# Kernel optimization log

Hardware: AMD Instinct MI355X
Metric: run time of the kernel (lower is better)

## Reference

```python
import jax, jax.numpy as jnp
import numpy as np

B, N = 4, 20                        # batch, qubits
L = int(np.ceil(np.log2(N)))        # 5 layers, one 4x4 generator each


def setup_inputs():
    key = jax.random.key(0)
    k1, k2, k3, k4 = jax.random.split(key, 4)
    psi_re = jax.random.normal(k1, (B, 2 ** N), dtype=jnp.float32)
    psi_im = jax.random.normal(k2, (B, 2 ** N), dtype=jnp.float32)
    nrm = jnp.sqrt(jnp.sum(psi_re ** 2 + psi_im ** 2, axis=1, keepdims=True))
    psi_re, psi_im = psi_re / nrm, psi_im / nrm   # normalized quantum state
    H_re = jax.random.normal(k3, (L, 4, 4), dtype=jnp.float32)
    H_im = jax.random.normal(k4, (L, 4, 4), dtype=jnp.float32)
    return {"psi_re": psi_re, "psi_im": psi_im, "H_re": H_re, "H_im": H_im}


def _make_unitary(A):
    # torch.matrix_exp(A - A^H): expm of an anti-Hermitian generator via eigh
    G = A - A.conj().T
    w, V = jnp.linalg.eigh(-1j * G)            # G = i * Hermitian
    return (V * jnp.exp(1j * w)) @ V.conj().T  # expm(G), unitary


def _apply_gate(T, U4, axes):
    # contract 4x4 gate (reshaped [2,2,2,2]) onto two qubit axes of tensor T
    T = jnp.tensordot(U4, T, axes=((2, 3), axes))
    return jnp.moveaxis(T, (0, 1), axes)


def _gate_pairs(nq):
    pairs = [(2 * i, 2 * i + 1) for i in range(nq // 2)]
    if nq > 2:
        pairs += [(2 * i + 1, (2 * i + 2) % nq) for i in range(nq // 2)]
    return pairs


def _forward(psi_re, psi_im, H_re, H_im):
    psi = (psi_re + 1j * psi_im).astype(jnp.complex64).reshape((B,) + (2,) * N)
    H = (H_re + 1j * H_im).astype(jnp.complex64)
    state, is_dm, nq = psi, False, N
    for layer in range(L):
        U = _make_unitary(H[layer]).reshape(2, 2, 2, 2)
        Uc = U.conj()
        # _2local_conv: brick pattern of the same 2-qubit gate
        for (a, b) in _gate_pairs(nq):
            state = _apply_gate(state, U, (1 + a, 1 + b))
            if is_dm:  # density matrix: also apply U* on bra axes
                state = _apply_gate(state, Uc, (1 + nq + a, 1 + nq + b))
        # _2local_pool: measuring qubits 0..nq//2-1 with index shifting removes
        # the even-indexed qubits -> partial trace over them
        if nq >= 2:
            traced = [2 * i for i in range(nq // 2)]
            kept = [q for q in range(nq) if q not in traced]
            t, k = len(traced), len(kept)
            if is_dm:
                perm = (0,) + tuple(1 + q for q in kept) + tuple(1 + q for q in traced) \
                     + tuple(1 + nq + q for q in kept) + tuple(1 + nq + q for q in traced)
                r = jnp.transpose(state, perm).reshape(B, 2 ** k, 2 ** t, 2 ** k, 2 ** t)
                state = jnp.einsum('bitjt->bij', r).reshape((B,) + (2,) * k + (2,) * k)
            else:
                perm = (0,) + tuple(1 + q for q in traced) + tuple(1 + q for q in kept)
                p = jnp.transpose(state, perm).reshape(B, 2 ** t, 2 ** k)
                state = jnp.einsum('bti,btj->bij', p, p.conj()).reshape((B,) + (2,) * k + (2,) * k)
                is_dm = True
            nq = k
    # final state.measure(0): reduced 1-qubit density matrix, take P(outcome 0)
    r = state.reshape(B, 2, 2 ** (nq - 1), 2, 2 ** (nq - 1))
    rho0 = jnp.einsum('birjr->bij', r)
    return rho0[:, 0, 0].real


def reference(psi_re, psi_im, H_re, H_im):
    return _forward(psi_re, psi_im, H_re, H_im)
```

## Files before the change

### kernel.cpp

```cpp
#include <hip/hip_runtime.h>
#include <math.h>


typedef float cpx __attribute__((ext_vector_type(2)));

__device__ __forceinline__ cpx mkc(float x, float y) { cpx r; r.x = x; r.y = y; return r; }

__device__ __forceinline__ cpx cmul(cpx a, cpx b) {
  cpx r = a.xx * b;
  return __builtin_elementwise_fma(mkc(-a.y, a.y), b.yx, r);
}
__device__ __forceinline__ cpx cmadd(cpx acc, cpx a, cpx b) {
  acc = __builtin_elementwise_fma(a.xx, b, acc);
  return __builtin_elementwise_fma(mkc(-a.y, a.y), b.yx, acc);
}
__device__ __forceinline__ cpx cmaddc(cpx acc, cpx a, cpx b) {
  acc = __builtin_elementwise_fma(a.xx, mkc(b.x, -b.y), acc);
  return __builtin_elementwise_fma(a.yy, b.yx, acc);
}

__device__ __forceinline__ int pad(int e) { return e + (e >> 4); }
__device__ __forceinline__ int ins(int x, int p) {
  return ((x >> p) << (p + 1)) | (x & ((1 << p) - 1));
}

#define S_STR 36
#define T_STR 1153

__device__ __forceinline__ void gate4(cpx& v0, cpx& v1, cpx& v2, cpx& v3,
                                      const cpx (&U)[16]) {
  cpx n0 = cmul(U[0], v0);  n0 = cmadd(n0, U[1], v1);  n0 = cmadd(n0, U[2], v2);  n0 = cmadd(n0, U[3], v3);
  cpx n1 = cmul(U[4], v0);  n1 = cmadd(n1, U[5], v1);  n1 = cmadd(n1, U[6], v2);  n1 = cmadd(n1, U[7], v3);
  cpx n2 = cmul(U[8], v0);  n2 = cmadd(n2, U[9], v1);  n2 = cmadd(n2, U[10], v2); n2 = cmadd(n2, U[11], v3);
  cpx n3 = cmul(U[12], v0); n3 = cmadd(n3, U[13], v1); n3 = cmadd(n3, U[14], v2); n3 = cmadd(n3, U[15], v3);
  v0 = n0; v1 = n1; v2 = n2; v3 = n3;
}

template <int NG>
__device__ __forceinline__ void gate16n(cpx (&v)[16], const cpx (&U)[16]) {
#pragma unroll
  for (int g = 0; g < 4; g++)
    gate4(v[g * 4 + 0], v[g * 4 + 1], v[g * 4 + 2], v[g * 4 + 3], U);
#pragma unroll
  for (int lo = 0; lo < 4; lo++)
    gate4(v[lo], v[lo + 4], v[lo + 8], v[lo + 12], U);
  if (NG == 3) {
#pragma unroll
    for (int b3 = 0; b3 < 2; b3++)
#pragma unroll
      for (int b0 = 0; b0 < 2; b0++) {
        int j = b3 * 8 + b0;
        gate4(v[j], v[j + 2], v[j + 4], v[j + 6], U);
      }
  }
}

__device__ __forceinline__ void apply_gate_tile13(cpx* t, const cpx (&U)[16],
                                                  int pa, int pb, int tid) {
  int p0 = pa < pb ? pa : pb;
  int p1 = pa < pb ? pb : pa;
  int m0 = (1 << p0) - 1, m1 = (1 << p1) - 1;
  int ia = 1 << pa, ib = 1 << pb;
#pragma unroll
  for (int g = tid; g < 2048; g += 512) {
    int idx = ((g & ~m0) << 1) | (g & m0);
    idx = ((idx & ~m1) << 1) | (idx & m1);
    int e0 = pad(idx), e1 = pad(idx | ib), e2 = pad(idx | ia), e3 = pad(idx | ia | ib);
    cpx v0 = t[e0], v1 = t[e1], v2 = t[e2], v3 = t[e3];
    gate4(v0, v1, v2, v3, U);
    t[e0] = v0; t[e1] = v1; t[e2] = v2; t[e3] = v3;
  }
}

template <int NG>
__device__ __forceinline__ void phase4_f(cpx* t, const cpx (&U)[16],
                                         int q0, int q1, int q2, int q3,
                                         int o0, int o1, int o2, int o3, int tid) {
  int idx = ins(ins(ins(ins(tid, q0), q1), q2), q3);
  cpx v[16];
#pragma unroll
  for (int j = 0; j < 16; j++) {
    int off = ((j & 1) ? o0 : 0) + ((j & 2) ? o1 : 0) + ((j & 4) ? o2 : 0) + ((j & 8) ? o3 : 0);
    v[j] = t[pad(idx + off)];
  }
  gate16n<NG>(v, U);
#pragma unroll
  for (int j = 0; j < 16; j++) {
    int off = ((j & 1) ? o0 : 0) + ((j & 2) ? o1 : 0) + ((j & 4) ? o2 : 0) + ((j & 8) ? o3 : 0);
    t[pad(idx + off)] = v[j];
  }
}

template <int NG>
__device__ __forceinline__ void phase4_pool(cpx* w, const cpx (&U)[16],
                                            int a_lo, int a_hi, int c_lo, int c_hi,
                                            int o0, int o1, int o2, int o3, int tid) {
  int uu = tid & 7, ss = (tid >> 3) & 7, t_lo = tid >> 6;
  int u = ins(ins(uu, a_lo), a_hi);
  int s = ins(ins(ss, c_lo), c_hi);
  int base = t_lo * T_STR + s * S_STR + u;
  cpx v[16];
#pragma unroll
  for (int j = 0; j < 16; j++) {
    int off = ((j & 1) ? o0 : 0) + ((j & 2) ? o1 : 0) + ((j & 4) ? o2 : 0) + ((j & 8) ? o3 : 0);
    v[j] = w[base + off];
  }
  gate16n<NG>(v, U);
#pragma unroll
  for (int j = 0; j < 16; j++) {
    int off = ((j & 1) ? o0 : 0) + ((j & 2) ? o1 : 0) + ((j & 4) ? o2 : 0) + ((j & 8) ? o3 : 0);
    w[base + off] = v[j];
  }
}

__device__ __forceinline__ void pool_p3(cpx* w, const cpx (&U)[16], int tid) {
#pragma unroll
  for (int it = 0; it < 2; it++) {
    int h = tid + it * 512;
    int t_lo = h & 7, ss = (h >> 3) & 15, uu = (h >> 7) & 7;
    int base = t_lo * T_STR + (ss << 1) * S_STR + (uu << 2);
    cpx v[8];
    v[0] = w[base];          v[1] = w[base + 1];
    v[4] = w[base + 2];      v[5] = w[base + 3];
    v[2] = w[base + S_STR];      v[3] = w[base + S_STR + 1];
    v[6] = w[base + S_STR + 2];  v[7] = w[base + S_STR + 3];
    gate4(v[0], v[1], v[2], v[3], U);
    gate4(v[4], v[5], v[6], v[7], U);
    gate4(v[0], v[2], v[4], v[6], U);
    gate4(v[1], v[3], v[5], v[7], U);
    w[base] = v[0];          w[base + 1] = v[1];
    w[base + 2] = v[4];      w[base + 3] = v[5];
    w[base + S_STR] = v[2];      w[base + S_STR + 1] = v[3];
    w[base + S_STR + 2] = v[6];  w[base + S_STR + 3] = v[7];
  }
}

__device__ __forceinline__ cpx expm16(const float* __restrict__ Hre,
                                      const float* __restrict__ Him,
                                      int l, int l16) {
  int r = l16 >> 2, c = l16 & 3;
  double tr = (double)Hre[l * 16 + r * 4 + c] - (double)Hre[l * 16 + c * 4 + r];
  double ti = (double)Him[l * 16 + r * 4 + c] + (double)Him[l * 16 + c * 4 + r];
  double a = sqrt(tr * tr + ti * ti);
  a += __shfl_xor(a, 1, 16);
  a += __shfl_xor(a, 2, 16);
  double nrm = fmax(a, __shfl_xor(a, 4, 16));
  nrm = fmax(nrm, __shfl_xor(nrm, 8, 16));
  int s = 0;
  while (nrm > 0.25 && s < 60) { nrm *= 0.5; s++; }
  double sc = ldexp(1.0, -s);
  tr *= sc; ti *= sc;
  double id = (r == c) ? 1.0 : 0.0;
  double er = id, ei = 0.0, pr = id, pi = 0.0;
  for (int k = 1; k <= 16; k++) {
    double qr = 0.0, qi = 0.0;
#pragma unroll
    for (int m = 0; m < 4; m++) {
      double pmr = __shfl(pr, r * 4 + m, 16);
      double pmi = __shfl(pi, r * 4 + m, 16);
      double tmr = __shfl(tr, m * 4 + c, 16);
      double tmi = __shfl(ti, m * 4 + c, 16);
      qr = fma(pmr, tmr, fma(-pmi, tmi, qr));
      qi = fma(pmr, tmi, fma(pmi, tmr, qi));
    }
    double inv = 1.0 / (double)k;
    pr = qr * inv; pi = qi * inv;
    er += pr; ei += pi;
  }
  for (int it = 0; it < s; it++) {
    double qr = 0.0, qi = 0.0;
#pragma unroll
    for (int m = 0; m < 4; m++) {
      double amr = __shfl(er, r * 4 + m, 16);
      double ami = __shfl(ei, r * 4 + m, 16);
      double bmr = __shfl(er, m * 4 + c, 16);
      double bmi = __shfl(ei, m * 4 + c, 16);
      qr = fma(amr, bmr, fma(-ami, bmi, qr));
      qi = fma(amr, bmi, fma(ami, bmr, qi));
    }
    er = qr; ei = qi;
  }
  return mkc((float)er, (float)ei);
}

__global__ __launch_bounds__(512, 4) void l0_pass1(const float* __restrict__ pre,
                                                   const float* __restrict__ pim,
                                                   const float* __restrict__ Hre,
                                                   const float* __restrict__ Him,
                                                   cpx* __restrict__ Umat,
                                                   cpx* __restrict__ state) {
  extern __shared__ cpx tile[];
  __shared__ cpx Ush[16];
  int tid = threadIdx.x;
  int bid = blockIdx.x;
  int b = bid >> 7, hi = bid & 127;
  size_t base = ((size_t)b << 20) | ((size_t)hi << 13);
  float4 re[4], im[4];
#pragma unroll
  for (int k = 0; k < 4; k++) {
    int e = (tid + (k << 9)) << 2;
    re[k] = *(const float4*)&pre[base + e];
    im[k] = *(const float4*)&pim[base + e];
  }
#pragma unroll
  for (int k = 0; k < 4; k++) {
    int e = (tid + (k << 9)) << 2;
    int d = pad(e);
    tile[d]     = mkc(re[k].x, im[k].x);
    tile[d + 1] = mkc(re[k].y, im[k].y);
    tile[d + 2] = mkc(re[k].z, im[k].z);
    tile[d + 3] = mkc(re[k].w, im[k].w);
  }
  {
    int wv = tid >> 6, g16 = (tid & 63) >> 4, l16 = tid & 15;
    int layer = (wv == 0) ? g16 : ((wv == 1 && g16 == 0) ? 4 : -1);
    if (layer == 0 || (bid == 0 && layer > 0)) {
      cpx ue = expm16(Hre, Him, layer, l16);
      if (layer == 0) Ush[l16] = ue;
      if (bid == 0) Umat[layer * 16 + l16] = ue;
    }
  }
  __syncthreads();
  cpx U[16];
#pragma unroll
  for (int k = 0; k < 16; k++) U[k] = Ush[k];
  phase4_f<3>(tile, U, 0, 1, 2, 3, 1, 2, 4, 8, tid);            __syncthreads();
  phase4_f<3>(tile, U, 4, 5, 6, 7, 16, 32, 64, 128, tid);       __syncthreads();
  phase4_f<3>(tile, U, 8, 9, 10, 11, 256, 512, 1024, 2048, tid);__syncthreads();
  phase4_f<2>(tile, U, 3, 4, 7, 8, 8, 16, 128, 256, tid);       __syncthreads();
  int hifix = ((hi & 1) << 16) | (((hi >> 1) & 1) << 6) | (((hi >> 2) & 1) << 17)
            | (((hi >> 3) & 1) << 5) | (((hi >> 4) & 1) << 18) | (((hi >> 5) & 1) << 7)
            | (((hi >> 6) & 1) << 19);
  size_t dbase = ((size_t)b << 20) | (unsigned)hifix;
  cpx x[16];
#pragma unroll
  for (int k = 0; k < 4; k++) {
    int src = pad((tid + (k << 9)) << 2);
    x[4 * k + 0] = tile[src];     x[4 * k + 1] = tile[src + 1];
    x[4 * k + 2] = tile[src + 2]; x[4 * k + 3] = tile[src + 3];
  }
#pragma unroll
  for (int k = 0; k < 4; k++) {
    int le = tid + (k << 9);
    int d = ((le & 1) << 2) | (((le >> 1) & 1) << 3) | (((le >> 2) & 1) << 8)
          | (((le >> 3) & 1) << 12) | (((le >> 4) & 1) << 10) | (((le >> 5) & 1) << 13)
          | (((le >> 6) & 1) << 9) | (((le >> 7) & 1) << 14) | (((le >> 8) & 1) << 11)
          | (((le >> 9) & 1) << 15) | (((le >> 10) & 1) << 4);
    float4* dst = (float4*)&state[dbase + d];
    dst[0] = make_float4(x[4 * k].x, x[4 * k].y, x[4 * k + 1].x, x[4 * k + 1].y);
    dst[1] = make_float4(x[4 * k + 2].x, x[4 * k + 2].y, x[4 * k + 3].x, x[4 * k + 3].y);
  }
}

__global__ __launch_bounds__(512, 4) void l0_pass2(const cpx* __restrict__ Umat,
                                                   cpx* __restrict__ state) {
  extern __shared__ cpx tile[];
  int tid = threadIdx.x;
  int bid = blockIdx.x;
  int b = bid >> 7, mid = bid & 127;
  size_t base = ((size_t)b << 20) | ((size_t)mid << 8);
  cpx U[16];
#pragma unroll
  for (int k = 0; k < 16; k++) U[k] = Umat[k];
  {
    float4 v[8];
#pragma unroll
    for (int k = 0; k < 8; k++) {
      int f = tid + (k << 9);
      int run = f >> 7, idx = f & 127;
      v[k] = *(const float4*)&state[base + ((size_t)run << 15) + ((size_t)idx << 1)];
    }
#pragma unroll
    for (int k = 0; k < 8; k++) {
      int f = tid + (k << 9);
      int d = pad((f >> 7) * 256 + (f & 127) * 2);
      tile[d] = mkc(v[k].x, v[k].y);
      tile[d + 1] = mkc(v[k].z, v[k].w);
    }
  }
  __syncthreads();
  phase4_f<3>(tile, U, 4, 6, 9, 10, 16, 512, 64, 1024, tid);    __syncthreads();
  phase4_f<3>(tile, U, 5, 7, 11, 12, 32, 2048, 128, 4096, tid); __syncthreads();
  phase4_f<2>(tile, U, 4, 5, 8, 10, 256, 16, 1024, 32, tid);    __syncthreads();
  apply_gate_tile13(tile, U, 0, 12, tid);                       __syncthreads();
  {
    cpx y[16];
#pragma unroll
    for (int k = 0; k < 8; k++) {
      int f = tid + (k << 9);
      int d = pad((f >> 7) * 256 + (f & 127) * 2);
      y[2 * k] = tile[d];
      y[2 * k + 1] = tile[d + 1];
    }
#pragma unroll
    for (int k = 0; k < 8; k++) {
      int f = tid + (k << 9);
      int run = f >> 7, idx = f & 127;
      size_t a = base + ((size_t)run << 15) + ((size_t)idx << 1);
      *(float4*)&state[a] = make_float4(y[2 * k].x, y[2 * k].y, y[2 * k + 1].x, y[2 * k + 1].y);
    }
  }
}

__global__ __launch_bounds__(512, 4) void pool_l1(const cpx* __restrict__ Umat,
                                                  const cpx* __restrict__ state,
                                                  float4* __restrict__ partial) {
  extern __shared__ cpx w[];
  int tid = threadIdx.x;
  int bid = blockIdx.x;
  int b = bid >> 7, thi = bid & 127;
  size_t base = ((size_t)b << 20) | ((size_t)thi << 13);
  cpx U[16];
#pragma unroll
  for (int k = 0; k < 16; k++) U[k] = Umat[16 + k];
  {
    float4 v[8];
#pragma unroll
    for (int k = 0; k < 8; k++) {
      int e = (tid + (k << 9)) << 1;
      v[k] = *(const float4*)&state[base + e];
    }
#pragma unroll
    for (int k = 0; k < 8; k++) {
      int e = (tid + (k << 9)) << 1;
      int u = (((e >> 8) & 1) << 1) | (((e >> 9) & 1) << 2) | (((e >> 4) & 1) << 3) | (((e >> 5) & 1) << 4);
      int s = ((e >> 2) & 1) | (((e >> 10) & 1) << 1) | (((e >> 11) & 1) << 2)
            | (((e >> 6) & 1) << 3) | (((e >> 7) & 1) << 4);
      int t = ((e >> 1) & 1) | (((e >> 3) & 1) << 1) | (((e >> 12) & 1) << 2);
      int c = t * T_STR + s * S_STR + u;
      w[c] = mkc(v[k].x, v[k].y);
      w[c + 1] = mkc(v[k].z, v[k].w);
    }
  }
  __syncthreads();
  phase4_pool<3>(w, U, 3, 4, 3, 4, 8, 8 * S_STR, 16, 16 * S_STR, tid); __syncthreads();
  phase4_pool<3>(w, U, 1, 2, 1, 2, 2, 2 * S_STR, 4, 4 * S_STR, tid);   __syncthreads();
  pool_p3(w, U, tid);                                                  __syncthreads();
  phase4_pool<2>(w, U, 0, 3, 2, 4, 4 * S_STR, 8, 16 * S_STR, 1, tid);  __syncthreads();
  int wv = tid >> 6, lane = tid & 63;
  int u0 = (lane >> 3) << 2, v0 = (lane & 7) << 2;
  cpx acc[4][4];
#pragma unroll
  for (int i = 0; i < 4; i++)
#pragma unroll
    for (int j = 0; j < 4; j++) acc[i][j] = mkc(0.f, 0.f);
  {
    int tb = wv * T_STR;
#pragma unroll 4
    for (int s = 0; s < 32; s++) {
      int row = tb + s * S_STR;
      cpx x[4], y[4];
#pragma unroll
      for (int i = 0; i < 4; i++) { x[i] = w[row + u0 + i]; y[i] = w[row + v0 + i]; }
#pragma unroll
      for (int i = 0; i < 4; i++)
#pragma unroll
        for (int j = 0; j < 4; j++) acc[i][j] = cmaddc(acc[i][j], x[i], y[j]);
    }
  }
  __syncthreads();
#pragma unroll
  for (int i = 0; i < 4; i++)
#pragma unroll
    for (int j = 0; j < 4; j++)
      w[wv * 1024 + (u0 + i) * 32 + (v0 + j)] = acc[i][j];
  __syncthreads();
  {
    cpx s0 = mkc(0.f, 0.f), s1 = mkc(0.f, 0.f);
#pragma unroll
    for (int k = 0; k < 8; k++) {
      s0 += w[k * 1024 + 2 * tid];
      s1 += w[k * 1024 + 2 * tid + 1];
    }
    partial[((size_t)bid << 9) | tid] = make_float4(s0.x, s0.y, s1.x, s1.y);
  }
}

__global__ __launch_bounds__(256) void finish(const cpx* __restrict__ Umat,
                                              const float4* __restrict__ accv,
                                              float* __restrict__ out) {
  __shared__ cpx rho[1024];
  __shared__ cpx r3s[64];
  __shared__ cpx r4s[16];
  int tid = threadIdx.x;
  int b = blockIdx.x;
  float4* rf = (float4*)rho;
  for (int f = tid; f < 512; f += 256) {
    float4 acc = make_float4(0.f, 0.f, 0.f, 0.f);
#pragma unroll 8
    for (int h = 0; h < 128; h++) {
      float4 v = accv[(size_t)(b * 128 + h) * 512 + f];
      acc.x += v.x; acc.y += v.y; acc.z += v.z; acc.w += v.w;
    }
    rf[f] = acc;
  }
  __syncthreads();

  cpx U[16], Uc[16];
#pragma unroll
  for (int k = 0; k < 16; k++) { U[k] = Umat[32 + k]; Uc[k] = mkc(U[k].x, -U[k].y); }
  const int gl2[4][2] = {{4,3},{2,1},{3,2},{1,0}};
#pragma unroll
  for (int gi = 0; gi < 4; gi++) {
    int pa = gl2[gi][0], pb = gl2[gi][1];
    int p0 = pa < pb ? pa : pb, p1 = pa < pb ? pb : pa;
    int m0 = (1 << p0) - 1, m1 = (1 << p1) - 1;
    int ia = 1 << pa, ib = 1 << pb;
    {
      int j = tid >> 3, g = tid & 7;
      int idx = ((g & ~m0) << 1) | (g & m0);
      idx = ((idx & ~m1) << 1) | (idx & m1);
      cpx v0 = rho[idx * 32 + j], v1 = rho[(idx | ib) * 32 + j];
      cpx v2 = rho[(idx | ia) * 32 + j], v3 = rho[(idx | ia | ib) * 32 + j];
      gate4(v0, v1, v2, v3, U);
      rho[idx * 32 + j] = v0; rho[(idx | ib) * 32 + j] = v1;
      rho[(idx | ia) * 32 + j] = v2; rho[(idx | ia | ib) * 32 + j] = v3;
    }
    __syncthreads();
    {
      int i = tid >> 3, g = tid & 7;
      int idx = ((g & ~m0) << 1) | (g & m0);
      idx = ((idx & ~m1) << 1) | (idx & m1);
      cpx v0 = rho[i * 32 + idx], v1 = rho[i * 32 + (idx | ib)];
      cpx v2 = rho[i * 32 + (idx | ia)], v3 = rho[i * 32 + (idx | ia | ib)];
      gate4(v0, v1, v2, v3, Uc);
      rho[i * 32 + idx] = v0; rho[i * 32 + (idx | ib)] = v1;
      rho[i * 32 + (idx | ia)] = v2; rho[i * 32 + (idx | ia | ib)] = v3;
    }
    __syncthreads();
  }
  if (tid < 64) {
    int u = tid >> 3, v = tid & 7;
    cpx acc = mkc(0.f, 0.f);
#pragma unroll
    for (int s = 0; s < 4; s++) {
      int iu = ((s >> 1) << 4) | ((u >> 2) << 3) | ((s & 1) << 2) | (((u >> 1) & 1) << 1) | (u & 1);
      int iv = ((s >> 1) << 4) | ((v >> 2) << 3) | ((s & 1) << 2) | (((v >> 1) & 1) << 1) | (v & 1);
      cpx x = rho[iu * 32 + iv];
      acc.x += x.x; acc.y += x.y;
    }
    r3s[u * 8 + v] = acc;
  }
  __syncthreads();

#pragma unroll
  for (int k = 0; k < 16; k++) { U[k] = Umat[48 + k]; Uc[k] = mkc(U[k].x, -U[k].y); }
  const int gl3[2][2] = {{2,1},{1,0}};
#pragma unroll
  for (int gi = 0; gi < 2; gi++) {
    int pa = gl3[gi][0], pb = gl3[gi][1];
    int p0 = pa < pb ? pa : pb, p1 = pa < pb ? pb : pa;
    int m0 = (1 << p0) - 1, m1 = (1 << p1) - 1;
    int ia = 1 << pa, ib = 1 << pb;
    if (tid < 16) {
      int j = tid >> 1, g = tid & 1;
      int idx = ((g & ~m0) << 1) | (g & m0);
      idx = ((idx & ~m1) << 1) | (idx & m1);
      cpx v0 = r3s[idx * 8 + j], v1 = r3s[(idx | ib) * 8 + j];
      cpx v2 = r3s[(idx | ia) * 8 + j], v3 = r3s[(idx | ia | ib) * 8 + j];
      gate4(v0, v1, v2, v3, U);
      r3s[idx * 8 + j] = v0; r3s[(idx | ib) * 8 + j] = v1;
      r3s[(idx | ia) * 8 + j] = v2; r3s[(idx | ia | ib) * 8 + j] = v3;
    }
    __syncthreads();
    if (tid < 16) {
      int i = tid >> 1, g = tid & 1;
      int idx = ((g & ~m0) << 1) | (g & m0);
      idx = ((idx & ~m1) << 1) | (idx & m1);
      cpx v0 = r3s[i * 8 + idx], v1 = r3s[i * 8 + (idx | ib)];
      cpx v2 = r3s[i * 8 + (idx | ia)], v3 = r3s[i * 8 + (idx | ia | ib)];
      gate4(v0, v1, v2, v3, Uc);
      r3s[i * 8 + idx] = v0; r3s[i * 8 + (idx | ib)] = v1;
      r3s[i * 8 + (idx | ia)] = v2; r3s[i * 8 + (idx | ia | ib)] = v3;
    }
    __syncthreads();
  }
  if (tid < 16) {
    int u = tid >> 2, v = tid & 3;
    cpx acc = mkc(0.f, 0.f);
#pragma unroll
    for (int s = 0; s < 2; s++) {
      cpx x = r3s[((s << 2) | u) * 8 + ((s << 2) | v)];
      acc.x += x.x; acc.y += x.y;
    }
    r4s[u * 4 + v] = acc;
  }
  __syncthreads();

#pragma unroll
  for (int k = 0; k < 16; k++) { U[k] = Umat[64 + k]; Uc[k] = mkc(U[k].x, -U[k].y); }
  if (tid < 4) {
    int j = tid;
    cpx v0 = r4s[0 * 4 + j], v1 = r4s[1 * 4 + j], v2 = r4s[2 * 4 + j], v3 = r4s[3 * 4 + j];
    gate4(v0, v1, v2, v3, U);
    r4s[0 * 4 + j] = v0; r4s[1 * 4 + j] = v1; r4s[2 * 4 + j] = v2; r4s[3 * 4 + j] = v3;
  }
  __syncthreads();
  if (tid < 4) {
    int i = tid;
    cpx v0 = r4s[i * 4 + 0], v1 = r4s[i * 4 + 1], v2 = r4s[i * 4 + 2], v3 = r4s[i * 4 + 3];
    gate4(v0, v1, v2, v3, Uc);
    r4s[i * 4 + 0] = v0; r4s[i * 4 + 1] = v1; r4s[i * 4 + 2] = v2; r4s[i * 4 + 3] = v3;
  }
  __syncthreads();
  if (tid == 0) out[b] = r4s[0].x + r4s[10].x;
}

extern "C" void kernel_launch(void* const* d_in, const int* in_sizes, int n_in,
                              void* d_out, int out_size, void* d_ws, size_t ws_size,
                              hipStream_t stream) {
  const float* psi_re = (const float*)d_in[0];
  const float* psi_im = (const float*)d_in[1];
  const float* H_re = (const float*)d_in[2];
  const float* H_im = (const float*)d_in[3];
  float* out = (float*)d_out;

  char* ws = (char*)d_ws;
  cpx* Umat = (cpx*)ws;
  cpx* state = (cpx*)(ws + 4096);
  float4* partial = (float4*)(ws + 4096 + ((size_t)1 << 25));

  const size_t LDS_L0 = 8704 * sizeof(cpx);
  const size_t LDS_POOL = 8 * T_STR * sizeof(cpx);

  hipLaunchKernelGGL(l0_pass1, dim3(512), dim3(512), LDS_L0, stream,
                     psi_re, psi_im, H_re, H_im, Umat, state);
  hipLaunchKernelGGL(l0_pass2, dim3(512), dim3(512), LDS_L0, stream,
                     (const cpx*)Umat, state);
  hipLaunchKernelGGL(pool_l1, dim3(512), dim3(512), LDS_POOL, stream,
                     (const cpx*)Umat, (const cpx*)state, partial);
  hipLaunchKernelGGL(finish, dim3(4), dim3(256), 0, stream,
                     (const cpx*)Umat, (const float4*)partial, out);
}
```

Before: 183.0 us.

## Split unitary computation into own kernel and use 1024-thread 3-qubit gate phases

Result: faster. 175.9 us (-3.9%).

```diff
diff --git a/kernel.cpp b/kernel.cpp
--- a/kernel.cpp
+++ b/kernel.cpp
@@ -55,14 +55,14 @@
   }
 }
 
-__device__ __forceinline__ void apply_gate_tile13(cpx* t, const cpx (&U)[16],
-                                                  int pa, int pb, int tid) {
+__device__ __forceinline__ void apply_gate_2it(cpx* t, const cpx (&U)[16],
+                                               int pa, int pb, int tid) {
   int p0 = pa < pb ? pa : pb;
   int p1 = pa < pb ? pb : pa;
   int m0 = (1 << p0) - 1, m1 = (1 << p1) - 1;
   int ia = 1 << pa, ib = 1 << pb;
 #pragma unroll
-  for (int g = tid; g < 2048; g += 512) {
+  for (int g = tid; g < 2048; g += 1024) {
     int idx = ((g & ~m0) << 1) | (g & m0);
     idx = ((idx & ~m1) << 1) | (idx & m1);
     int e0 = pad(idx), e1 = pad(idx | ib), e2 = pad(idx | ia), e3 = pad(idx | ia | ib);
@@ -72,21 +72,23 @@
   }
 }
 
-template <int NG>
-__device__ __forceinline__ void phase4_f(cpx* t, const cpx (&U)[16],
-                                         int q0, int q1, int q2, int q3,
-                                         int o0, int o1, int o2, int o3, int tid) {
-  int idx = ins(ins(ins(ins(tid, q0), q1), q2), q3);
-  cpx v[16];
-#pragma unroll
-  for (int j = 0; j < 16; j++) {
-    int off = ((j & 1) ? o0 : 0) + ((j & 2) ? o1 : 0) + ((j & 4) ? o2 : 0) + ((j & 8) ? o3 : 0);
+__device__ __forceinline__ void phase3_eo(cpx* t, const cpx (&U)[16],
+                                          int q0, int q1, int q2,
+                                          int o0, int o1, int o2, int tid) {
+  int idx = ins(ins(ins(tid, q0), q1), q2);
+  cpx v[8];
+#pragma unroll
+  for (int j = 0; j < 8; j++) {
+    int off = ((j & 1) ? o0 : 0) + ((j & 2) ? o1 : 0) + ((j & 4) ? o2 : 0);
     v[j] = t[pad(idx + off)];
   }
-  gate16n<NG>(v, U);
-#pragma unroll
-  for (int j = 0; j < 16; j++) {
-    int off = ((j & 1) ? o0 : 0) + ((j & 2) ? o1 : 0) + ((j & 4) ? o2 : 0) + ((j & 8) ? o3 : 0);
+  gate4(v[0], v[2], v[4], v[6], U);
+  gate4(v[1], v[3], v[5], v[7], U);
+  gate4(v[0], v[1], v[2], v[3], U);
+  gate4(v[4], v[5], v[6], v[7], U);
+#pragma unroll
+  for (int j = 0; j < 8; j++) {
+    int off = ((j & 1) ? o0 : 0) + ((j & 2) ? o1 : 0) + ((j & 4) ? o2 : 0);
     t[pad(idx + off)] = v[j];
   }
 }
@@ -183,65 +185,65 @@
   return mkc((float)er, (float)ei);
 }
 
-__global__ __launch_bounds__(512, 4) void l0_pass1(const float* __restrict__ pre,
-                                                   const float* __restrict__ pim,
-                                                   const float* __restrict__ Hre,
-                                                   const float* __restrict__ Him,
-                                                   cpx* __restrict__ Umat,
-                                                   cpx* __restrict__ state) {
+__global__ __launch_bounds__(128) void compute_U(const float* __restrict__ Hre,
+                                                 const float* __restrict__ Him,
+                                                 cpx* __restrict__ Umat) {
+  int tid = threadIdx.x;
+  if (tid < 80) {
+    int layer = tid >> 4, l16 = tid & 15;
+    Umat[layer * 16 + l16] = expm16(Hre, Him, layer, l16);
+  }
+}
+
+__global__ __launch_bounds__(1024, 8) void l0_pass1(const float* __restrict__ pre,
+                                                    const float* __restrict__ pim,
+                                                    const cpx* __restrict__ Umat,
+                                                    cpx* __restrict__ state) {
   extern __shared__ cpx tile[];
-  __shared__ cpx Ush[16];
   int tid = threadIdx.x;
   int bid = blockIdx.x;
   int b = bid >> 7, hi = bid & 127;
   size_t base = ((size_t)b << 20) | ((size_t)hi << 13);
-  float4 re[4], im[4];
-#pragma unroll
-  for (int k = 0; k < 4; k++) {
-    int e = (tid + (k << 9)) << 2;
+  float4 re[2], im[2];
+#pragma unroll
+  for (int k = 0; k < 2; k++) {
+    int e = (tid + (k << 10)) << 2;
     re[k] = *(const float4*)&pre[base + e];
     im[k] = *(const float4*)&pim[base + e];
   }
 #pragma unroll
-  for (int k = 0; k < 4; k++) {
-    int e = (tid + (k << 9)) << 2;
+  for (int k = 0; k < 2; k++) {
+    int e = (tid + (k << 10)) << 2;
     int d = pad(e);
     tile[d]     = mkc(re[k].x, im[k].x);
     tile[d + 1] = mkc(re[k].y, im[k].y);
     tile[d + 2] = mkc(re[k].z, im[k].z);
     tile[d + 3] = mkc(re[k].w, im[k].w);
   }
-  {
-    int wv = tid >> 6, g16 = (tid & 63) >> 4, l16 = tid & 15;
-    int layer = (wv == 0) ? g16 : ((wv == 1 && g16 == 0) ? 4 : -1);
-    if (layer == 0 || (bid == 0 && layer > 0)) {
-      cpx ue = expm16(Hre, Him, layer, l16);
-      if (layer == 0) Ush[l16] = ue;
-      if (bid == 0) Umat[layer * 16 + l16] = ue;
-    }
-  }
-  __syncthreads();
   cpx U[16];
 #pragma unroll
-  for (int k = 0; k < 16; k++) U[k] = Ush[k];
-  phase4_f<3>(tile, U, 0, 1, 2, 3, 1, 2, 4, 8, tid);            __syncthreads();
-  phase4_f<3>(tile, U, 4, 5, 6, 7, 16, 32, 64, 128, tid);       __syncthreads();
-  phase4_f<3>(tile, U, 8, 9, 10, 11, 256, 512, 1024, 2048, tid);__syncthreads();
-  phase4_f<2>(tile, U, 3, 4, 7, 8, 8, 16, 128, 256, tid);       __syncthreads();
+  for (int k = 0; k < 16; k++) U[k] = Umat[k];
+  __syncthreads();
+  apply_gate_2it(tile, U, 1, 0, tid);                 __syncthreads();
+  phase3_eo(tile, U, 1, 2, 3, 2, 4, 8, tid);          __syncthreads();
+  phase3_eo(tile, U, 3, 4, 5, 8, 16, 32, tid);        __syncthreads();
+  phase3_eo(tile, U, 5, 6, 7, 32, 64, 128, tid);      __syncthreads();
+  phase3_eo(tile, U, 7, 8, 9, 128, 256, 512, tid);    __syncthreads();
+  phase3_eo(tile, U, 9, 10, 11, 512, 1024, 2048, tid);__syncthreads();
   int hifix = ((hi & 1) << 16) | (((hi >> 1) & 1) << 6) | (((hi >> 2) & 1) << 17)
             | (((hi >> 3) & 1) << 5) | (((hi >> 4) & 1) << 18) | (((hi >> 5) & 1) << 7)
             | (((hi >> 6) & 1) << 19);
   size_t dbase = ((size_t)b << 20) | (unsigned)hifix;
-  cpx x[16];
-#pragma unroll
-  for (int k = 0; k < 4; k++) {
-    int src = pad((tid + (k << 9)) << 2);
+  cpx x[8];
+#pragma unroll
+  for (int k = 0; k < 2; k++) {
+    int src = pad((tid + (k << 10)) << 2);
     x[4 * k + 0] = tile[src];     x[4 * k + 1] = tile[src + 1];
     x[4 * k + 2] = tile[src + 2]; x[4 * k + 3] = tile[src + 3];
   }
 #pragma unroll
-  for (int k = 0; k < 4; k++) {
-    int le = tid + (k << 9);
+  for (int k = 0; k < 2; k++) {
+    int le = tid + (k << 10);
     int d = ((le & 1) << 2) | (((le >> 1) & 1) << 3) | (((le >> 2) & 1) << 8)
           | (((le >> 3) & 1) << 12) | (((le >> 4) & 1) << 10) | (((le >> 5) & 1) << 13)
           | (((le >> 6) & 1) << 9) | (((le >> 7) & 1) << 14) | (((le >> 8) & 1) << 11)
@@ -252,8 +254,8 @@
   }
 }
 
-__global__ __launch_bounds__(512, 4) void l0_pass2(const cpx* __restrict__ Umat,
-                                                   cpx* __restrict__ state) {
+__global__ __launch_bounds__(1024, 8) void l0_pass2(const cpx* __restrict__ Umat,
+                                                    cpx* __restrict__ state) {
   extern __shared__ cpx tile[];
   int tid = threadIdx.x;
   int bid = blockIdx.x;
@@ -263,38 +265,39 @@
 #pragma unroll
   for (int k = 0; k < 16; k++) U[k] = Umat[k];
   {
-    float4 v[8];
-#pragma unroll
-    for (int k = 0; k < 8; k++) {
-      int f = tid + (k << 9);
+    float4 v[4];
+#pragma unroll
+    for (int k = 0; k < 4; k++) {
+      int f = tid + (k << 10);
       int run = f >> 7, idx = f & 127;
       v[k] = *(const float4*)&state[base + ((size_t)run << 15) + ((size_t)idx << 1)];
     }
 #pragma unroll
-    for (int k = 0; k < 8; k++) {
-      int f = tid + (k << 9);
+    for (int k = 0; k < 4; k++) {
+      int f = tid + (k << 10);
       int d = pad((f >> 7) * 256 + (f & 127) * 2);
       tile[d] = mkc(v[k].x, v[k].y);
       tile[d + 1] = mkc(v[k].z, v[k].w);
     }
   }
   __syncthreads();
-  phase4_f<3>(tile, U, 4, 6, 9, 10, 16, 512, 64, 1024, tid);    __syncthreads();
-  phase4_f<3>(tile, U, 5, 7, 11, 12, 32, 2048, 128, 4096, tid); __syncthreads();
-  phase4_f<2>(tile, U, 4, 5, 8, 10, 256, 16, 1024, 32, tid);    __syncthreads();
-  apply_gate_tile13(tile, U, 0, 12, tid);                       __syncthreads();
+  phase3_eo(tile, U, 4, 8, 9, 256, 16, 512, tid);     __syncthreads();
+  phase3_eo(tile, U, 6, 9, 10, 512, 64, 1024, tid);   __syncthreads();
+  phase3_eo(tile, U, 5, 10, 11, 1024, 32, 2048, tid); __syncthreads();
+  phase3_eo(tile, U, 7, 11, 12, 2048, 128, 4096, tid);__syncthreads();
+  apply_gate_2it(tile, U, 0, 12, tid);                __syncthreads();
   {
-    cpx y[16];
-#pragma unroll
-    for (int k = 0; k < 8; k++) {
-      int f = tid + (k << 9);
+    cpx y[8];
+#pragma unroll
+    for (int k = 0; k < 4; k++) {
+      int f = tid + (k << 10);
       int d = pad((f >> 7) * 256 + (f & 127) * 2);
       y[2 * k] = tile[d];
       y[2 * k + 1] = tile[d + 1];
     }
 #pragma unroll
-    for (int k = 0; k < 8; k++) {
-      int f = tid + (k << 9);
+    for (int k = 0; k < 4; k++) {
+      int f = tid + (k << 10);
       int run = f >> 7, idx = f & 127;
       size_t a = base + ((size_t)run << 15) + ((size_t)idx << 1);
       *(float4*)&state[a] = make_float4(y[2 * k].x, y[2 * k].y, y[2 * k + 1].x, y[2 * k + 1].y);
@@ -523,9 +526,10 @@
   const size_t LDS_L0 = 8704 * sizeof(cpx);
   const size_t LDS_POOL = 8 * T_STR * sizeof(cpx);
 
-  hipLaunchKernelGGL(l0_pass1, dim3(512), dim3(512), LDS_L0, stream,
-                     psi_re, psi_im, H_re, H_im, Umat, state);
-  hipLaunchKernelGGL(l0_pass2, dim3(512), dim3(512), LDS_L0, stream,
+  hipLaunchKernelGGL(compute_U, dim3(1), dim3(128), 0, stream, H_re, H_im, Umat);
+  hipLaunchKernelGGL(l0_pass1, dim3(512), dim3(1024), LDS_L0, stream,
+                     psi_re, psi_im, (const cpx*)Umat, state);
+  hipLaunchKernelGGL(l0_pass2, dim3(512), dim3(1024), LDS_L0, stream,
                      (const cpx*)Umat, state);
   hipLaunchKernelGGL(pool_l1, dim3(512), dim3(512), LDS_POOL, stream,
                      (const cpx*)Umat, (const cpx*)state, partial);
```
